# Performance work log

Hardware: AMD Instinct MI355X
Metric: run time of the kernel (lower is better)

## Reference

```python
import jax, jax.numpy as jnp
import numpy as np

SIZE = 1024
CODE_DIM = 256
B, H, W = 32, 32, 32


def setup_inputs() -> dict:
    key = jax.random.key(0)
    k1, k2 = jax.random.split(key)
    z = jax.random.normal(k1, (B, CODE_DIM, H, W), dtype=jnp.float32)
    embeddings = jax.random.normal(k2, (SIZE, CODE_DIM), dtype=jnp.float32)
    return {"z": z, "embeddings": embeddings}


def reference(z, embeddings):
    b, c, h, w = z.shape  # c == code_dim
    # (b, h, w, c) -> (N, c)
    flat = jnp.transpose(z, (0, 2, 3, 1)).reshape(-1, c)
    d = (
        jnp.sum(flat * flat, axis=-1, keepdims=True)
        - 2.0 * (flat @ embeddings.T)
        + jnp.sum(embeddings * embeddings, axis=-1)
    )
    idx = jnp.argmin(d, axis=-1)  # (N,)
    quantized = embeddings[idx].reshape(b, h, w, c)
    quantized = jnp.transpose(quantized, (0, 3, 1, 2))  # (b, c, h, w)
    straight_through = jax.lax.stop_gradient(quantized - z) + z
    return quantized, straight_through, idx.reshape(b, h, w)
```

## Files before the change

### kernel.cpp

```cpp
#include <hip/hip_runtime.h>

#define NPTS   32768
#define NCODES 1024
#define DIM    256
#define HWSZ   1024
#define CHW    (DIM*HWSZ)
#define QSZ    8388608

typedef __attribute__((ext_vector_type(8))) short short8;
typedef __attribute__((ext_vector_type(4))) float f32x4;

__device__ __forceinline__ void gload16(const void* g, void* l) {
    __builtin_amdgcn_global_load_lds((const __attribute__((address_space(1))) void*)g,
                                     (__attribute__((address_space(3))) void*)l,
                                     16, 0, 0);
}

__device__ __forceinline__ unsigned bf16_rne(float f) {
    unsigned u = __float_as_uint(f);
    return (u + 0x7fffu + ((u >> 16) & 1u)) >> 16;
}

__global__ void k_prep(const float* __restrict__ z, const float* __restrict__ emb,
                       short* __restrict__ Xh, short* __restrict__ Xl,
                       short* __restrict__ Eh, short* __restrict__ El,
                       float* __restrict__ e2) {
    int tid = threadIdx.x;
    if (blockIdx.x >= 1024) {
        int lane = tid & 63, w = tid >> 6;
        int k = (blockIdx.x - 1024) * 4 + w;
        const float4 v = *reinterpret_cast<const float4*>(emb + k * DIM + lane * 4);
        float f[4] = {v.x, v.y, v.z, v.w};
        short h[4], l[4];
        double s = 0.0;
        #pragma unroll
        for (int i = 0; i < 4; ++i) {
            unsigned hb = bf16_rne(f[i]);
            float hf = __uint_as_float(hb << 16);
            h[i] = (short)hb;
            l[i] = (short)bf16_rne(f[i] - hf);
            s += (double)f[i] * f[i];
        }
        *reinterpret_cast<short4*>(Eh + k * DIM + lane * 4) = make_short4(h[0], h[1], h[2], h[3]);
        *reinterpret_cast<short4*>(El + k * DIM + lane * 4) = make_short4(l[0], l[1], l[2], l[3]);
        #pragma unroll
        for (int m = 32; m >= 1; m >>= 1) s += __shfl_xor(s, m);
        if (lane == 0) e2[k] = (float)s;
        return;
    }
    __shared__ float T[64][33];
    int blk = blockIdx.x;
    int b  = blk >> 5;
    int ht = blk & 31;
    int hw0 = ht * 32;
    int n0  = b * HWSZ + hw0;
    int hq = tid & 7, cr = tid >> 3;
    int wp = tid >> 3, wc = tid & 7;
    const float* zp = z + b * CHW;
    #pragma unroll
    for (int cc = 0; cc < 4; ++cc) {
        int c0 = cc * 64;
        if (cc) __syncthreads();
        #pragma unroll
        for (int p = 0; p < 2; ++p) {
            int c = p * 32 + cr;
            float4 v = *reinterpret_cast<const float4*>(zp + (c0 + c) * HWSZ + hw0 + hq * 4);
            T[c][hq * 4 + 0] = v.x; T[c][hq * 4 + 1] = v.y;
            T[c][hq * 4 + 2] = v.z; T[c][hq * 4 + 3] = v.w;
        }
        __syncthreads();
        short8 hv, lv;
        #pragma unroll
        for (int k = 0; k < 8; ++k) {
            float f = T[wc * 8 + k][wp];
            unsigned hb = bf16_rne(f);
            float hf = __uint_as_float(hb << 16);
            hv[k] = (short)hb;
            lv[k] = (short)bf16_rne(f - hf);
        }
        *reinterpret_cast<short8*>(Xh + (n0 + wp) * DIM + c0 + wc * 8) = hv;
        *reinterpret_cast<short8*>(Xl + (n0 + wp) * DIM + c0 + wc * 8) = lv;
    }
}

__launch_bounds__(256, 4)
__global__ void k_dist(const short* __restrict__ Xh, const short* __restrict__ Xl,
                       const short* __restrict__ Eh, const short* __restrict__ El,
                       const float* __restrict__ e2, float* __restrict__ minv,
                       int* __restrict__ mini) {
    __shared__ __align__(16) short Ah[4096];
    __shared__ __align__(16) short Al[4096];
    __shared__ __align__(16) short Bh[4096];
    __shared__ __align__(16) short Bl[4096];
    __shared__ float sv[2][128];
    __shared__ int   si[2][128];

    const int tid = threadIdx.x;
    const int pt = blockIdx.x & 255;
    const int ct = blockIdx.x >> 8;
    const int n0 = pt * 128;
    const int c0 = ct * 128;

    const int w = tid >> 6, lane = tid & 63;
    const int wr = w >> 1, wc = w & 1;
    const int m16 = lane & 15, quad = lane >> 4;

    f32x4 acc[4][4];
    #pragma unroll
    for (int i = 0; i < 4; ++i)
        #pragma unroll
        for (int j = 0; j < 4; ++j) acc[i][j] = (f32x4){0.f, 0.f, 0.f, 0.f};

    const int r   = lane >> 2;
    const int swz = (((lane & 3) - ((lane >> 3) & 3)) & 3) * 8;
    const int ldsoff0 = (w * 16) * 64;
    const int ldsoff1 = (64 + w * 16) * 64;
    const int arow0 = (n0 + w * 16 + r) * DIM;
    const int arow1 = (n0 + 64 + w * 16 + r) * DIM;
    const int brow0 = (c0 + w * 16 + r) * DIM;
    const int brow1 = (c0 + 64 + w * 16 + r) * DIM;

    const int pq = ((quad + (m16 >> 1)) & 3) * 8;

    for (int t = 0; t < 8; ++t) {
        const int koff = t * 32 + swz;
        __syncthreads();
        gload16(Xh + arow0 + koff, (char*)Ah + ldsoff0);
        gload16(Xh + arow1 + koff, (char*)Ah + ldsoff1);
        gload16(Xl + arow0 + koff, (char*)Al + ldsoff0);
        gload16(Xl + arow1 + koff, (char*)Al + ldsoff1);
        gload16(Eh + brow0 + koff, (char*)Bh + ldsoff0);
        gload16(Eh + brow1 + koff, (char*)Bh + ldsoff1);
        gload16(El + brow0 + koff, (char*)Bl + ldsoff0);
        gload16(El + brow1 + koff, (char*)Bl + ldsoff1);
        __syncthreads();

        short8 ah[4], al[4], bh[4], bl[4];
        #pragma unroll
        for (int i = 0; i < 4; ++i) {
            int ar = (wr * 64 + i * 16 + m16) * 32 + pq;
            ah[i] = *(const short8*)&Ah[ar];
            al[i] = *(const short8*)&Al[ar];
        }
        #pragma unroll
        for (int j = 0; j < 4; ++j) {
            int br = (wc * 64 + j * 16 + m16) * 32 + pq;
            bh[j] = *(const short8*)&Bh[br];
            bl[j] = *(const short8*)&Bl[br];
        }
        #pragma unroll
        for (int i = 0; i < 4; ++i)
            #pragma unroll
            for (int j = 0; j < 4; ++j)
                acc[i][j] = __builtin_amdgcn_mfma_f32_16x16x32_bf16(ah[i], bh[j], acc[i][j], 0, 0, 0);
        #pragma unroll
        for (int i = 0; i < 4; ++i)
            #pragma unroll
            for (int j = 0; j < 4; ++j)
                acc[i][j] = __builtin_amdgcn_mfma_f32_16x16x32_bf16(al[i], bh[j], acc[i][j], 0, 0, 0);
        #pragma unroll
        for (int i = 0; i < 4; ++i)
            #pragma unroll
            for (int j = 0; j < 4; ++j)
                acc[i][j] = __builtin_amdgcn_mfma_f32_16x16x32_bf16(ah[i], bl[j], acc[i][j], 0, 0, 0);
    }

    float ecol[4];
    #pragma unroll
    for (int j = 0; j < 4; ++j) ecol[j] = e2[c0 + wc * 64 + j * 16 + m16];

    #pragma unroll
    for (int i = 0; i < 4; ++i) {
        #pragma unroll
        for (int rr = 0; rr < 4; ++rr) {
            float best = 3.4e38f; int bi = 0;
            #pragma unroll
            for (int j = 0; j < 4; ++j) {
                float d = fmaf(-2.f, acc[i][j][rr], ecol[j]);
                int code = c0 + wc * 64 + j * 16 + m16;
                if (d < best) { best = d; bi = code; }
            }
            #pragma unroll
            for (int m = 1; m < 16; m <<= 1) {
                float ov = __shfl_xor(best, m);
                int   oi = __shfl_xor(bi, m);
                if (ov < best || (ov == best && oi < bi)) { best = ov; bi = oi; }
            }
            if (m16 == 0) {
                int p = wr * 64 + i * 16 + quad * 4 + rr;
                sv[wc][p] = best; si[wc][p] = bi;
            }
        }
    }
    __syncthreads();
    if (tid < 128) {
        float v0 = sv[0][tid]; int i0 = si[0][tid];
        float v1 = sv[1][tid]; int i1 = si[1][tid];
        if (v1 < v0) { v0 = v1; i0 = i1; }
        minv[ct * NPTS + n0 + tid] = v0;
        mini[ct * NPTS + n0 + tid] = i0;
    }
}

__global__ void k_out(const float* __restrict__ z, const float* __restrict__ emb,
                      const float* __restrict__ minv, const int* __restrict__ mini,
                      float* __restrict__ out) {
    __shared__ float Q[32][257];
    __shared__ int sbi[32];
    int n0 = blockIdx.x * 32;
    int tid = threadIdx.x;
    if (tid < 32) {
        int n = n0 + tid;
        float bv = minv[n]; int bi = mini[n];
        #pragma unroll
        for (int g = 1; g < 8; ++g) {
            float v = minv[g * NPTS + n]; int ii = mini[g * NPTS + n];
            if (v < bv) { bv = v; bi = ii; }
        }
        sbi[tid] = bi;
        out[2 * QSZ + n] = (float)bi;
    }
    __syncthreads();
    {
        int pt = tid >> 3, co = tid & 7;
        const float* ep = emb + sbi[pt] * DIM;
        #pragma unroll
        for (int j = 0; j < 8; ++j) {
            int c = j * 32 + co * 4;
            float4 v = *reinterpret_cast<const float4*>(ep + c);
            Q[pt][c] = v.x; Q[pt][c + 1] = v.y; Q[pt][c + 2] = v.z; Q[pt][c + 3] = v.w;
        }
    }
    __syncthreads();
    int hq = tid & 7, cr = tid >> 3;
    int b = n0 >> 10, hw0 = (n0 & 1023) + hq * 4;
    #pragma unroll
    for (int it = 0; it < 8; ++it) {
        int c = it * 32 + cr;
        int off = b * CHW + c * HWSZ + hw0;
        float4 zv = *reinterpret_cast<const float4*>(z + off);
        float4 q = make_float4(Q[hq * 4 + 0][c], Q[hq * 4 + 1][c],
                               Q[hq * 4 + 2][c], Q[hq * 4 + 3][c]);
        *reinterpret_cast<float4*>(out + off) = q;
        float4 st = make_float4((q.x - zv.x) + zv.x, (q.y - zv.y) + zv.y,
                                (q.z - zv.z) + zv.z, (q.w - zv.w) + zv.w);
        *reinterpret_cast<float4*>(out + QSZ + off) = st;
    }
}

extern "C" void kernel_launch(void* const* d_in, const int* in_sizes, int n_in,
                              void* d_out, int out_size, void* d_ws, size_t ws_size,
                              hipStream_t stream) {
    const float* z   = (const float*)d_in[0];
    const float* emb = (const float*)d_in[1];
    float* out = (float*)d_out;
    float* ws  = (float*)d_ws;

    short* Eh   = (short*)ws;
    short* El   = (short*)(ws + 131072);
    float* e2   = ws + 262144;
    float* minv = ws + 263168;
    int*   mini = (int*)(ws + 525312);

    short* Xh = (short*)out;
    short* Xl = (short*)(out + 4194304);

    hipLaunchKernelGGL(k_prep, dim3(1280), dim3(256), 0, stream, z, emb, Xh, Xl, Eh, El, e2);
    hipLaunchKernelGGL(k_dist, dim3(2048), dim3(256), 0, stream, Xh, Xl, Eh, El, e2, minv, mini);
    hipLaunchKernelGGL(k_out,  dim3(1024), dim3(256), 0, stream, z, emb, minv, mini, out);
}
```

Measured before the change: 165.8 us.

## Merge per-tile argmin results with 64-bit atomicMin and split prep/out grids

Each distance tile now folds its candidate into a per-point packed (order-preserving distance key, index) word with a 64-bit atomicMin. This replaces writing eight partial min arrays and re-reducing them in the output kernel. The prep kernel initialises the packed array and splits each point tile over two channel halves, doubling the block count. The output kernel likewise splits channels across two blocks. Atomics add contention across the eight code tiles, and ties now resolve to the smaller index.

```diff
diff --git a/kernel.cpp b/kernel.cpp
--- a/kernel.cpp
+++ b/kernel.cpp
@@ -21,14 +21,23 @@
     return (u + 0x7fffu + ((u >> 16) & 1u)) >> 16;
 }
 
+__device__ __forceinline__ unsigned long long pack_di(float d, int code) {
+    unsigned u = __float_as_uint(d);
+    unsigned key = u ^ ((unsigned)((int)u >> 31) | 0x80000000u);
+    return ((unsigned long long)key << 32) | (unsigned)code;
+}
+
 __global__ void k_prep(const float* __restrict__ z, const float* __restrict__ emb,
                        short* __restrict__ Xh, short* __restrict__ Xl,
                        short* __restrict__ Eh, short* __restrict__ El,
-                       float* __restrict__ e2) {
+                       float* __restrict__ e2, unsigned long long* __restrict__ win) {
     int tid = threadIdx.x;
-    if (blockIdx.x >= 1024) {
+    if (blockIdx.x >= 2048) {
+        int eb = blockIdx.x - 2048;
+        int widx = eb * 256 + tid;
+        if (widx < NPTS) win[widx] = ~0ull;
         int lane = tid & 63, w = tid >> 6;
-        int k = (blockIdx.x - 1024) * 4 + w;
+        int k = eb * 4 + w;
         const float4 v = *reinterpret_cast<const float4*>(emb + k * DIM + lane * 4);
         float f[4] = {v.x, v.y, v.z, v.w};
         short h[4], l[4];
@@ -50,17 +59,19 @@
     }
     __shared__ float T[64][33];
     int blk = blockIdx.x;
-    int b  = blk >> 5;
-    int ht = blk & 31;
+    int b   = blk >> 6;
+    int rem = blk & 63;
+    int ht  = rem >> 1;
+    int ch  = rem & 1;
     int hw0 = ht * 32;
     int n0  = b * HWSZ + hw0;
     int hq = tid & 7, cr = tid >> 3;
     int wp = tid >> 3, wc = tid & 7;
     const float* zp = z + b * CHW;
     #pragma unroll
-    for (int cc = 0; cc < 4; ++cc) {
-        int c0 = cc * 64;
-        if (cc) __syncthreads();
+    for (int cc2 = 0; cc2 < 2; ++cc2) {
+        int c0 = (ch * 2 + cc2) * 64;
+        if (cc2) __syncthreads();
         #pragma unroll
         for (int p = 0; p < 2; ++p) {
             int c = p * 32 + cr;
@@ -86,8 +97,7 @@
 __launch_bounds__(256, 4)
 __global__ void k_dist(const short* __restrict__ Xh, const short* __restrict__ Xl,
                        const short* __restrict__ Eh, const short* __restrict__ El,
-                       const float* __restrict__ e2, float* __restrict__ minv,
-                       int* __restrict__ mini) {
+                       const float* __restrict__ e2, unsigned long long* __restrict__ win) {
     __shared__ __align__(16) short Ah[4096];
     __shared__ __align__(16) short Al[4096];
     __shared__ __align__(16) short Bh[4096];
@@ -197,35 +207,31 @@
         float v0 = sv[0][tid]; int i0 = si[0][tid];
         float v1 = sv[1][tid]; int i1 = si[1][tid];
         if (v1 < v0) { v0 = v1; i0 = i1; }
-        minv[ct * NPTS + n0 + tid] = v0;
-        mini[ct * NPTS + n0 + tid] = i0;
+        atomicMin(win + n0 + tid, pack_di(v0, i0));
     }
 }
 
 __global__ void k_out(const float* __restrict__ z, const float* __restrict__ emb,
-                      const float* __restrict__ minv, const int* __restrict__ mini,
+                      const unsigned long long* __restrict__ win,
                       float* __restrict__ out) {
-    __shared__ float Q[32][257];
+    __shared__ float Q[32][129];
     __shared__ int sbi[32];
-    int n0 = blockIdx.x * 32;
+    int blk = blockIdx.x;
+    int n0 = (blk >> 1) * 32;
+    int ch = blk & 1;
     int tid = threadIdx.x;
     if (tid < 32) {
         int n = n0 + tid;
-        float bv = minv[n]; int bi = mini[n];
-        #pragma unroll
-        for (int g = 1; g < 8; ++g) {
-            float v = minv[g * NPTS + n]; int ii = mini[g * NPTS + n];
-            if (v < bv) { bv = v; bi = ii; }
-        }
+        int bi = (int)(unsigned)(win[n] & 0xFFFFFFFFull);
         sbi[tid] = bi;
-        out[2 * QSZ + n] = (float)bi;
+        if (ch == 0) out[2 * QSZ + n] = (float)bi;
     }
     __syncthreads();
     {
         int pt = tid >> 3, co = tid & 7;
-        const float* ep = emb + sbi[pt] * DIM;
-        #pragma unroll
-        for (int j = 0; j < 8; ++j) {
+        const float* ep = emb + sbi[pt] * DIM + ch * 128;
+        #pragma unroll
+        for (int j = 0; j < 4; ++j) {
             int c = j * 32 + co * 4;
             float4 v = *reinterpret_cast<const float4*>(ep + c);
             Q[pt][c] = v.x; Q[pt][c + 1] = v.y; Q[pt][c + 2] = v.z; Q[pt][c + 3] = v.w;
@@ -235,12 +241,13 @@
     int hq = tid & 7, cr = tid >> 3;
     int b = n0 >> 10, hw0 = (n0 & 1023) + hq * 4;
     #pragma unroll
-    for (int it = 0; it < 8; ++it) {
-        int c = it * 32 + cr;
+    for (int it = 0; it < 4; ++it) {
+        int cl = it * 32 + cr;
+        int c  = ch * 128 + cl;
         int off = b * CHW + c * HWSZ + hw0;
         float4 zv = *reinterpret_cast<const float4*>(z + off);
-        float4 q = make_float4(Q[hq * 4 + 0][c], Q[hq * 4 + 1][c],
-                               Q[hq * 4 + 2][c], Q[hq * 4 + 3][c]);
+        float4 q = make_float4(Q[hq * 4 + 0][cl], Q[hq * 4 + 1][cl],
+                               Q[hq * 4 + 2][cl], Q[hq * 4 + 3][cl]);
         *reinterpret_cast<float4*>(out + off) = q;
         float4 st = make_float4((q.x - zv.x) + zv.x, (q.y - zv.y) + zv.y,
                                 (q.z - zv.z) + zv.z, (q.w - zv.w) + zv.w);
@@ -259,13 +266,12 @@
     short* Eh   = (short*)ws;
     short* El   = (short*)(ws + 131072);
     float* e2   = ws + 262144;
-    float* minv = ws + 263168;
-    int*   mini = (int*)(ws + 525312);
+    unsigned long long* win = (unsigned long long*)(ws + 263168);
 
     short* Xh = (short*)out;
     short* Xl = (short*)(out + 4194304);
 
-    hipLaunchKernelGGL(k_prep, dim3(1280), dim3(256), 0, stream, z, emb, Xh, Xl, Eh, El, e2);
-    hipLaunchKernelGGL(k_dist, dim3(2048), dim3(256), 0, stream, Xh, Xl, Eh, El, e2, minv, mini);
-    hipLaunchKernelGGL(k_out,  dim3(1024), dim3(256), 0, stream, z, emb, minv, mini, out);
-}
+    hipLaunchKernelGGL(k_prep, dim3(2304), dim3(256), 0, stream, z, emb, Xh, Xl, Eh, El, e2, win);
+    hipLaunchKernelGGL(k_dist, dim3(2048), dim3(256), 0, stream, Xh, Xl, Eh, El, e2, win);
+    hipLaunchKernelGGL(k_out,  dim3(2048), dim3(256), 0, stream, z, emb, win, out);
+}
```

Result: no change. 164.9 us (-0.6%).
